# Optimization experiments

Hardware: AMD Instinct MI355X
Metric: run time of the kernel (lower is better)

## Reference

```python
import jax, jax.numpy as jnp
import numpy as np

B, T, D, H, E = 4, 512, 2048, 1024, 2


def setup_inputs() -> dict:
    key = jax.random.key(0)
    k = jax.random.split(key, 4)
    return {
        "x": jax.random.normal(k[0], (B, T, D), jnp.float32),
        "Wg": jax.random.normal(k[1], (D, E), jnp.float32) / np.float32(np.sqrt(D)),
        "W1": jax.random.normal(k[2], (E, D, H), jnp.float32) / np.float32(np.sqrt(D)),
        "b1": jnp.zeros((E, H), jnp.float32),
        "W2": jax.random.normal(k[3], (E, H, D), jnp.float32) / np.float32(np.sqrt(H)),
        "b2": jnp.zeros((E, D), jnp.float32),
    }


def reference(x, Wg, W1, b1, W2, b2):
    # --- Top1 gate: bias-free linear -> softmax -> argmax routing ---
    logits = jnp.einsum('btd,de->bte', x, Wg)            # [B,T,E]
    probs = jax.nn.softmax(logits, axis=-1)
    idx = jnp.argmax(probs, axis=-1)                     # [B,T] chosen expert
    gate = jnp.max(probs, axis=-1)                       # [B,T] top-1 prob
    # --- expert FFN (identity activation): fc1 -> fc2, batched per expert ---
    h = jnp.einsum('btd,edh->ebth', x, W1) + b1[:, None, None, :]   # [E,B,T,H]
    y = jnp.einsum('ebth,ehd->ebtd', h, W2) + b2[:, None, None, :]  # [E,B,T,D]
    # --- combine: select routed expert output, scale by gate value ---
    sel = jax.nn.one_hot(idx, E, dtype=x.dtype) * gate[..., None]   # [B,T,E]
    moe_out = jnp.einsum('ebtd,bte->btd', y, sel)                   # [B,T,D]
    # --- model head: sum over model_dim, log_softmax over tokens ---
    return jax.nn.log_softmax(jnp.sum(moe_out, axis=2), axis=1)     # [B,T]
```

## Files before the change

kernel.cpp:

```cpp
#include <hip/hip_runtime.h>
#include <math.h>

#define B_ 4
#define T_ 512
#define D_ 2048
#define H_ 1024
#define E_ 2

#define LD4(p) (*reinterpret_cast<const float4*>(p))


__device__ __forceinline__ float waveReduceSum(float v) {
    #pragma unroll
    for (int o = 32; o > 0; o >>= 1) v += __shfl_down(v, o, 64);
    return v;
}

__global__ __launch_bounds__(256) void k_w2sum(const float* __restrict__ W2,
                                               float* __restrict__ w2s) {
    int gw   = (blockIdx.x * 256 + threadIdx.x) >> 6;
    int lane = threadIdx.x & 63;
    const float* p0 = W2 + (size_t)(2 * gw) * D_;
    const float* p1 = p0 + D_;
    float a0 = 0.f, a1 = 0.f;
    #pragma unroll
    for (int k = 0; k < D_ / 256; ++k) {
        float4 u = LD4(p0 + (lane + k * 64) * 4);
        float4 w = LD4(p1 + (lane + k * 64) * 4);
        a0 += (u.x + u.y) + (u.z + u.w);
        a1 += (w.x + w.y) + (w.z + w.w);
    }
    #pragma unroll
    for (int o = 32; o > 0; o >>= 1) {
        a0 += __shfl_down(a0, o, 64);
        a1 += __shfl_down(a1, o, 64);
    }
    if (lane == 0) {
        w2s[2 * gw]     = a0;
        w2s[2 * gw + 1] = a1;
    }
}

__global__ __launch_bounds__(256) void k_vred(const float* __restrict__ W1,
                                              const float* __restrict__ w2s,
                                              const float* __restrict__ b1,
                                              const float* __restrict__ b2,
                                              float* __restrict__ v,
                                              float* __restrict__ c) {
    if (blockIdx.x >= 512) {
        __shared__ float lds[4];
        int e = blockIdx.x - 512;
        float acc = 0.f;
        for (int i = threadIdx.x; i < H_; i += 256) acc += b1[e * H_ + i] * w2s[e * H_ + i];
        for (int i = threadIdx.x; i < D_; i += 256) acc += b2[e * D_ + i];
        acc = waveReduceSum(acc);
        if ((threadIdx.x & 63) == 0) lds[threadIdx.x >> 6] = acc;
        __syncthreads();
        if (threadIdx.x == 0) c[e] = lds[0] + lds[1] + lds[2] + lds[3];
        return;
    }
    int gw   = (blockIdx.x * 256 + threadIdx.x) >> 6;
    int lane = threadIdx.x & 63;
    int row0 = 2 * gw;
    int e    = row0 >> 11;
    const float* p0 = W1 + (size_t)row0 * H_;
    const float* p1 = p0 + H_;
    const float* w  = w2s + e * H_;
    float a0 = 0.f, a1 = 0.f;
    #pragma unroll
    for (int k = 0; k < H_ / 256; ++k) {
        float4 wa = LD4(w  + (lane + k * 64) * 4);
        float4 u  = LD4(p0 + (lane + k * 64) * 4);
        float4 t  = LD4(p1 + (lane + k * 64) * 4);
        a0 += u.x * wa.x + u.y * wa.y + u.z * wa.z + u.w * wa.w;
        a1 += t.x * wa.x + t.y * wa.y + t.z * wa.z + t.w * wa.w;
    }
    #pragma unroll
    for (int o = 32; o > 0; o >>= 1) {
        a0 += __shfl_down(a0, o, 64);
        a1 += __shfl_down(a1, o, 64);
    }
    if (lane == 0) {
        v[row0]     = a0;
        v[row0 + 1] = a1;
    }
}

__global__ __launch_bounds__(256) void k_token(const float* __restrict__ x,
                                               const float* __restrict__ Wg,
                                               const float* __restrict__ v,
                                               const float* __restrict__ c,
                                               float* __restrict__ s) {
    int lane = threadIdx.x & 63;
    int bt   = (blockIdx.x * 256 + threadIdx.x) >> 6;
    const float* xp = x + (size_t)bt * D_;
    float g0 = 0.f, g1 = 0.f, d0 = 0.f, d1 = 0.f;
    #pragma unroll
    for (int k = 0; k < D_ / 256; ++k) {
        int i = (lane + k * 64) * 4;
        float4 xv = LD4(xp + i);
        float4 v0 = LD4(v + i);
        float4 v1 = LD4(v + D_ + i);
        float4 wa = LD4(Wg + 2 * i);
        float4 wb = LD4(Wg + 2 * i + 4);
        g0 += xv.x * wa.x + xv.y * wa.z + xv.z * wb.x + xv.w * wb.z;
        g1 += xv.x * wa.y + xv.y * wa.w + xv.z * wb.y + xv.w * wb.w;
        d0 += xv.x * v0.x + xv.y * v0.y + xv.z * v0.z + xv.w * v0.w;
        d1 += xv.x * v1.x + xv.y * v1.y + xv.z * v1.z + xv.w * v1.w;
    }
    #pragma unroll
    for (int o = 32; o > 0; o >>= 1) {
        g0 += __shfl_down(g0, o, 64);
        g1 += __shfl_down(g1, o, 64);
        d0 += __shfl_down(d0, o, 64);
        d1 += __shfl_down(d1, o, 64);
    }
    if (lane == 0) {
        int e = (g1 > g0) ? 1 : 0;
        float m  = fmaxf(g0, g1);
        float p0 = expf(g0 - m), p1 = expf(g1 - m);
        float gate = ((e == 0) ? p0 : p1) / (p0 + p1);
        float dot  = (e == 0) ? d0 : d1;
        s[bt] = gate * (dot + c[e]);
    }
}

__global__ void k_lsm(const float* __restrict__ s, float* __restrict__ out) {
    __shared__ float lds[8];
    int b = blockIdx.x;
    int t = threadIdx.x;
    int lane = t & 63, wid = t >> 6;
    float val = s[b * T_ + t];

    float m = val;
    #pragma unroll
    for (int o = 1; o < 64; o <<= 1) m = fmaxf(m, __shfl_xor(m, o, 64));
    if (lane == 0) lds[wid] = m;
    __syncthreads();
    m = lds[0];
    #pragma unroll
    for (int w = 1; w < 8; ++w) m = fmaxf(m, lds[w]);
    __syncthreads();

    float ex = expf(val - m);
    float sum = ex;
    #pragma unroll
    for (int o = 1; o < 64; o <<= 1) sum += __shfl_xor(sum, o, 64);
    if (lane == 0) lds[wid] = sum;
    __syncthreads();
    sum = 0.f;
    #pragma unroll
    for (int w = 0; w < 8; ++w) sum += lds[w];

    out[b * T_ + t] = val - m - logf(sum);
}

extern "C" void kernel_launch(void* const* d_in, const int* in_sizes, int n_in,
                              void* d_out, int out_size, void* d_ws, size_t ws_size,
                              hipStream_t stream) {
    (void)in_sizes; (void)n_in; (void)out_size; (void)ws_size;
    const float* x  = (const float*)d_in[0];
    const float* Wg = (const float*)d_in[1];
    const float* W1 = (const float*)d_in[2];
    const float* b1 = (const float*)d_in[3];
    const float* W2 = (const float*)d_in[4];
    const float* b2 = (const float*)d_in[5];
    float* out = (float*)d_out;

    float* ws  = (float*)d_ws;
    float* w2s = ws;
    float* v   = ws + 2048;
    float* c   = ws + 6144;
    float* s   = ws + 6160;

    k_w2sum<<<256, 256, 0, stream>>>(W2, w2s);
    k_vred <<<514, 256, 0, stream>>>(W1, w2s, b1, b2, v, c);
    k_token<<<512, 256, 0, stream>>>(x, Wg, v, c, s);
    k_lsm  <<<B_,  512, 0, stream>>>(s, out);
}
```

Measured before the change: 23.24 us.

## Fuse W1 reduction with token dot products via D-chunked partial sums

Replaces the separate v-vector reduction and per-token gate/dot kernels with one kernel. Each block computes a 32-wide chunk of v and immediately applies it, with the gate weights, to all tokens, writing partial sums. A final combine kernel sums the 64 partials, computes the bias constants, applies top-1 gating and performs the log-softmax, removing one launch and a dependency. The cost is extra partial-sum traffic, strided x access per thread, and a combine stage that runs on only four blocks.

```diff
diff --git a/kernel.cpp b/kernel.cpp
--- a/kernel.cpp
+++ b/kernel.cpp
@@ -6,6 +6,8 @@
 #define D_ 2048
 #define H_ 1024
 #define E_ 2
+#define DC_ 32
+#define NDC_ 64
 
 #define LD4(p) (*reinterpret_cast<const float4*>(p))
 
@@ -41,118 +43,118 @@
     }
 }
 
-__global__ __launch_bounds__(256) void k_vred(const float* __restrict__ W1,
+__global__ __launch_bounds__(256) void k_part(const float* __restrict__ W1,
+                                              const float* __restrict__ Wg,
+                                              const float* __restrict__ x,
+                                              const float* __restrict__ w2s,
+                                              float* __restrict__ A,
+                                              float* __restrict__ G) {
+    __shared__ float lv[DC_], lw[DC_];
+    int e    = blockIdx.x >> 7;
+    int dc   = (blockIdx.x >> 1) & 63;
+    int half = blockIdx.x & 1;
+    int tid  = threadIdx.x;
+    int lane = tid & 63, wid = tid >> 6;
+
+    const float* w = w2s + e * H_;
+    #pragma unroll
+    for (int r = 0; r < 8; ++r) {
+        int j = wid * 8 + r;
+        const float* p = W1 + ((size_t)e * D_ + dc * DC_ + j) * H_;
+        float acc = 0.f;
+        #pragma unroll
+        for (int k = 0; k < H_ / 256; ++k) {
+            float4 a = LD4(p + (lane + k * 64) * 4);
+            float4 b = LD4(w + (lane + k * 64) * 4);
+            acc += a.x * b.x + a.y * b.y + a.z * b.z + a.w * b.w;
+        }
+        acc = waveReduceSum(acc);
+        if (lane == 0) lv[j] = acc;
+    }
+    if (tid < DC_) lw[tid] = Wg[(dc * DC_ + tid) * E_ + e];
+    __syncthreads();
+
+    float* Arow = A + ((size_t)e * NDC_ + dc) * (B_ * T_);
+    float* Grow = G + ((size_t)e * NDC_ + dc) * (B_ * T_);
+    #pragma unroll 2
+    for (int r = 0; r < 4; ++r) {
+        int bt = half * 1024 + r * 256 + tid;
+        const float* xp = x + (size_t)bt * D_ + dc * DC_;
+        float z = 0.f, g = 0.f;
+        #pragma unroll
+        for (int q = 0; q < 8; ++q) {
+            float4 xv = LD4(xp + q * 4);
+            z += xv.x * lv[q*4+0] + xv.y * lv[q*4+1] + xv.z * lv[q*4+2] + xv.w * lv[q*4+3];
+            g += xv.x * lw[q*4+0] + xv.y * lw[q*4+1] + xv.z * lw[q*4+2] + xv.w * lw[q*4+3];
+        }
+        Arow[bt] = z;
+        Grow[bt] = g;
+    }
+}
+
+__global__ __launch_bounds__(512) void k_comb(const float* __restrict__ A,
+                                              const float* __restrict__ G,
                                               const float* __restrict__ w2s,
                                               const float* __restrict__ b1,
                                               const float* __restrict__ b2,
-                                              float* __restrict__ v,
-                                              float* __restrict__ c) {
-    if (blockIdx.x >= 512) {
-        __shared__ float lds[4];
-        int e = blockIdx.x - 512;
+                                              float* __restrict__ out) {
+    __shared__ float red[8];
+    __shared__ float cc[E_];
+    int b = blockIdx.x, tid = threadIdx.x;
+    int lane = tid & 63, wid = tid >> 6;
+
+    #pragma unroll
+    for (int e = 0; e < E_; ++e) {
         float acc = 0.f;
-        for (int i = threadIdx.x; i < H_; i += 256) acc += b1[e * H_ + i] * w2s[e * H_ + i];
-        for (int i = threadIdx.x; i < D_; i += 256) acc += b2[e * D_ + i];
+        for (int i = tid; i < H_; i += 512) acc += b1[e * H_ + i] * w2s[e * H_ + i];
+        for (int i = tid; i < D_; i += 512) acc += b2[e * D_ + i];
         acc = waveReduceSum(acc);
-        if ((threadIdx.x & 63) == 0) lds[threadIdx.x >> 6] = acc;
+        if (lane == 0) red[wid] = acc;
         __syncthreads();
-        if (threadIdx.x == 0) c[e] = lds[0] + lds[1] + lds[2] + lds[3];
-        return;
+        if (tid == 0) {
+            float t = 0.f;
+            #pragma unroll
+            for (int w2 = 0; w2 < 8; ++w2) t += red[w2];
+            cc[e] = t;
+        }
+        __syncthreads();
     }
-    int gw   = (blockIdx.x * 256 + threadIdx.x) >> 6;
-    int lane = threadIdx.x & 63;
-    int row0 = 2 * gw;
-    int e    = row0 >> 11;
-    const float* p0 = W1 + (size_t)row0 * H_;
-    const float* p1 = p0 + H_;
-    const float* w  = w2s + e * H_;
-    float a0 = 0.f, a1 = 0.f;
-    #pragma unroll
-    for (int k = 0; k < H_ / 256; ++k) {
-        float4 wa = LD4(w  + (lane + k * 64) * 4);
-        float4 u  = LD4(p0 + (lane + k * 64) * 4);
-        float4 t  = LD4(p1 + (lane + k * 64) * 4);
-        a0 += u.x * wa.x + u.y * wa.y + u.z * wa.z + u.w * wa.w;
-        a1 += t.x * wa.x + t.y * wa.y + t.z * wa.z + t.w * wa.w;
+
+    int bt = b * T_ + tid;
+    float z0 = 0.f, z1 = 0.f, g0 = 0.f, g1 = 0.f;
+    #pragma unroll 8
+    for (int dc = 0; dc < NDC_; ++dc) {
+        z0 += A[(size_t)(0 * NDC_ + dc) * (B_ * T_) + bt];
+        z1 += A[(size_t)(1 * NDC_ + dc) * (B_ * T_) + bt];
+        g0 += G[(size_t)(0 * NDC_ + dc) * (B_ * T_) + bt];
+        g1 += G[(size_t)(1 * NDC_ + dc) * (B_ * T_) + bt];
     }
-    #pragma unroll
-    for (int o = 32; o > 0; o >>= 1) {
-        a0 += __shfl_down(a0, o, 64);
-        a1 += __shfl_down(a1, o, 64);
-    }
-    if (lane == 0) {
-        v[row0]     = a0;
-        v[row0 + 1] = a1;
-    }
-}
-
-__global__ __launch_bounds__(256) void k_token(const float* __restrict__ x,
-                                               const float* __restrict__ Wg,
-                                               const float* __restrict__ v,
-                                               const float* __restrict__ c,
-                                               float* __restrict__ s) {
-    int lane = threadIdx.x & 63;
-    int bt   = (blockIdx.x * 256 + threadIdx.x) >> 6;
-    const float* xp = x + (size_t)bt * D_;
-    float g0 = 0.f, g1 = 0.f, d0 = 0.f, d1 = 0.f;
-    #pragma unroll
-    for (int k = 0; k < D_ / 256; ++k) {
-        int i = (lane + k * 64) * 4;
-        float4 xv = LD4(xp + i);
-        float4 v0 = LD4(v + i);
-        float4 v1 = LD4(v + D_ + i);
-        float4 wa = LD4(Wg + 2 * i);
-        float4 wb = LD4(Wg + 2 * i + 4);
-        g0 += xv.x * wa.x + xv.y * wa.z + xv.z * wb.x + xv.w * wb.z;
-        g1 += xv.x * wa.y + xv.y * wa.w + xv.z * wb.y + xv.w * wb.w;
-        d0 += xv.x * v0.x + xv.y * v0.y + xv.z * v0.z + xv.w * v0.w;
-        d1 += xv.x * v1.x + xv.y * v1.y + xv.z * v1.z + xv.w * v1.w;
-    }
-    #pragma unroll
-    for (int o = 32; o > 0; o >>= 1) {
-        g0 += __shfl_down(g0, o, 64);
-        g1 += __shfl_down(g1, o, 64);
-        d0 += __shfl_down(d0, o, 64);
-        d1 += __shfl_down(d1, o, 64);
-    }
-    if (lane == 0) {
-        int e = (g1 > g0) ? 1 : 0;
-        float m  = fmaxf(g0, g1);
-        float p0 = expf(g0 - m), p1 = expf(g1 - m);
-        float gate = ((e == 0) ? p0 : p1) / (p0 + p1);
-        float dot  = (e == 0) ? d0 : d1;
-        s[bt] = gate * (dot + c[e]);
-    }
-}
-
-__global__ void k_lsm(const float* __restrict__ s, float* __restrict__ out) {
-    __shared__ float lds[8];
-    int b = blockIdx.x;
-    int t = threadIdx.x;
-    int lane = t & 63, wid = t >> 6;
-    float val = s[b * T_ + t];
+    int e = (g1 > g0) ? 1 : 0;
+    float m0 = fmaxf(g0, g1);
+    float p0 = expf(g0 - m0), p1 = expf(g1 - m0);
+    float gate = ((e == 0) ? p0 : p1) / (p0 + p1);
+    float val  = gate * (((e == 0) ? z0 : z1) + cc[e]);
 
     float m = val;
     #pragma unroll
     for (int o = 1; o < 64; o <<= 1) m = fmaxf(m, __shfl_xor(m, o, 64));
-    if (lane == 0) lds[wid] = m;
+    if (lane == 0) red[wid] = m;
     __syncthreads();
-    m = lds[0];
+    m = red[0];
     #pragma unroll
-    for (int w = 1; w < 8; ++w) m = fmaxf(m, lds[w]);
+    for (int w2 = 1; w2 < 8; ++w2) m = fmaxf(m, red[w2]);
     __syncthreads();
 
-    float ex = expf(val - m);
-    float sum = ex;
+    float sum = expf(val - m);
     #pragma unroll
     for (int o = 1; o < 64; o <<= 1) sum += __shfl_xor(sum, o, 64);
-    if (lane == 0) lds[wid] = sum;
+    if (lane == 0) red[wid] = sum;
     __syncthreads();
     sum = 0.f;
     #pragma unroll
-    for (int w = 0; w < 8; ++w) sum += lds[w];
+    for (int w2 = 0; w2 < 8; ++w2) sum += red[w2];
 
-    out[b * T_ + t] = val - m - logf(sum);
+    out[bt] = val - m - logf(sum);
 }
 
 extern "C" void kernel_launch(void* const* d_in, const int* in_sizes, int n_in,
@@ -169,12 +171,10 @@
 
     float* ws  = (float*)d_ws;
     float* w2s = ws;
-    float* v   = ws + 2048;
-    float* c   = ws + 6144;
-    float* s   = ws + 6160;
+    float* A   = ws + 2048;
+    float* G   = ws + 2048 + 262144;
 
     k_w2sum<<<256, 256, 0, stream>>>(W2, w2s);
-    k_vred <<<514, 256, 0, stream>>>(W1, w2s, b1, b2, v, c);
-    k_token<<<512, 256, 0, stream>>>(x, Wg, v, c, s);
-    k_lsm  <<<B_,  512, 0, stream>>>(s, out);
+    k_part <<<256, 256, 0, stream>>>(W1, Wg, x, w2s, A, G);
+    k_comb <<<B_,  512, 0, stream>>>(A, G, w2s, b1, b2, out);
 }
```

Result: slower. 36.73 us (+58.0%).
